# Kernel optimization log

Hardware: AMD Instinct MI355X
Metric: run time of the kernel (lower is better)

Reference implementation:

```python
import jax, jax.numpy as jnp
import numpy as np
from jax import lax

THRESH = 0.8
LENS = 0.4
DECAY = 0.2
LOG_SIG_MIN, LOG_SIG_MAX = -20.0, 2.0
WINS = 15

@jax.custom_vjp
def act_fun(x):
    return (x > THRESH).astype(x.dtype)

def _act_fwd(x):
    return act_fun(x), x

def _act_bwd(x, g):
    return (g * (jnp.abs(x - THRESH) < LENS).astype(g.dtype),)

act_fun.defvjp(_act_fwd, _act_bwd)

B, NIN, HID, NACT = 2048, 512, 1024, 32

def _xavier(key, out_d, in_d):
    lim = jnp.sqrt(6.0 / (in_d + out_d)).astype(jnp.float32)
    return jax.random.uniform(key, (out_d, in_d), jnp.float32, -lim, lim)

def setup_inputs() -> dict:
    key = jax.random.key(0)
    ks = jax.random.split(key, 12)
    inp = {
        'state': jax.random.normal(ks[0], (B, 5, NIN), jnp.float32),
        'w1': _xavier(ks[1], HID, NIN), 'b1': jnp.zeros((HID,), jnp.float32),
        'w2': _xavier(ks[2], HID, NIN), 'b2': jnp.zeros((HID,), jnp.float32),
        'w3': _xavier(ks[3], HID, NIN), 'b3': jnp.zeros((HID,), jnp.float32),
        'wl': _xavier(ks[4], 1, 3), 'bl': jnp.zeros((1,), jnp.float32),
        'w11': _xavier(ks[5], HID, 4 * HID), 'b11': jnp.zeros((HID,), jnp.float32),
        'w12': _xavier(ks[6], HID, HID), 'b12': jnp.zeros((HID,), jnp.float32),
        'w21': _xavier(ks[7], HID, 4 * HID), 'b21': jnp.zeros((HID,), jnp.float32),
        'w22': _xavier(ks[8], HID, HID), 'b22': jnp.zeros((HID,), jnp.float32),
        'wm': _xavier(ks[9], NACT, HID), 'bm': jnp.zeros((NACT,), jnp.float32),
        'ws': _xavier(ks[10], NACT, HID), 'bs': jnp.zeros((NACT,), jnp.float32),
    }
    return inp

def _policy_forward(state, w1, b1, w2, b2, w3, b3, wl, bl,
                    w11, b11, w12, b12, w21, b21, w22, b22, wm, bm, ws, bs):
    batch = state.shape[0]
    hid = w1.shape[0]
    seq = jnp.repeat(state, 3, axis=1)
    mem0 = jnp.zeros((batch, hid, 4), state.dtype)
    sp0 = jnp.zeros((batch, hid, 4), state.dtype)

    def step(carry, x_t):
        mem, spike = carry
        i1 = x_t @ w1.T + b1  # [B, HID]
        i2 = x_t @ w2.T + b2
        i3 = x_t @ w3.T + b3
        inner = jnp.einsum('bck,k->bc', mem[:, :, :3], wl[0]) + bl[0]
        inp_all = jnp.stack([i1, i2, i3, inner], axis=-1)  # [B, HID, 4]
        mem1 = mem * DECAY * (1.0 - spike) + inp_all
        sp1 = act_fun(mem1)
        return (mem1, sp1), sp1

    _, spikes = lax.scan(step, (mem0, sp0), jnp.swapaxes(seq, 0, 1))  # [T,B,HID,4]
    spikes = jnp.transpose(spikes, (1, 0, 2, 3)).reshape(batch, WINS, hid * 4)
    x = jnp.mean(spikes, axis=1)  # [B, 4*HID]

    x1 = jax.nn.relu(x @ w11.T + b11)
    x1 = jax.nn.relu(x1 @ w12.T + b12)
    mean = x1 @ wm.T + bm

    x2 = jax.nn.relu(x @ w21.T + b21)
    x2 = jax.nn.relu(x2 @ w22.T + b22)
    log_std = jnp.clip(x2 @ ws.T + bs, LOG_SIG_MIN, LOG_SIG_MAX)
    return mean, log_std

def reference(state, w1, b1, w2, b2, w3, b3, wl, bl,
              w11, b11, w12, b12, w21, b21, w22, b22, wm, bm, ws, bs):
    return _policy_forward(state, w1, b1, w2, b2, w3, b3, wl, bl,
                           w11, b11, w12, b12, w21, b21, w22, b22, wm, bm, ws, bs)
```

## Files before the change

kernel.cpp:

```cpp
#include <hip/hip_runtime.h>
#include <cstddef>
#include <cstdint>

#define THRESH 0.8f
#define DECAY  0.2f

typedef unsigned short ushort_t;
typedef __attribute__((ext_vector_type(8))) short bf16x8;
typedef __attribute__((ext_vector_type(4))) float f32x4;

__device__ __forceinline__ ushort_t f2bf(float f) {
    union { float f; unsigned u; } v; v.f = f;
    unsigned r = v.u + 0x7FFFu + ((v.u >> 16) & 1u);
    return (ushort_t)(r >> 16);
}
__device__ __forceinline__ float bf2f(ushort_t h) {
    union { unsigned u; float f; } v; v.u = ((unsigned)h) << 16;
    return v.f;
}
__device__ __forceinline__ float blo(unsigned u) {
    union { unsigned x; float f; } v; v.x = u << 16; return v.f;
}
__device__ __forceinline__ float bhi(unsigned u) {
    union { unsigned x; float f; } v; v.x = u & 0xFFFF0000u; return v.f;
}

__device__ __forceinline__ void gload16(const void* g, void* l) {
    __builtin_amdgcn_global_load_lds(
        (const __attribute__((address_space(1))) void*)g,
        (__attribute__((address_space(3))) void*)l,
        16, 0, 0);
}

__global__ __launch_bounds__(512) void cur_gemm512(
    const ushort_t* __restrict__ Ah, const ushort_t* __restrict__ Al,
    const ushort_t* __restrict__ Wh, const ushort_t* __restrict__ Wl,
    const float* __restrict__ bias, float* __restrict__ C,
    int K, int ldc)
{
    __shared__ ushort_t sA[2][128 * 32];
    __shared__ ushort_t sW[2][128 * 32];

    const int t = threadIdx.x;
    const int mBase = blockIdx.x * 128;
    const int nBase = blockIdx.y * 128;

    const int lane = t & 63;
    const int wv = t >> 6;
    const int wm = (wv & 1) * 64;
    const int wn = (wv >> 1) * 32;
    const int fr = lane & 15;
    const int fq = lane >> 4;

    const int r0 = t >> 2;
    const int cc = (t & 3) * 8;

    f32x4 acc[4][2];
#pragma unroll
    for (int i = 0; i < 4; i++)
#pragma unroll
        for (int j = 0; j < 2; j++) {
            f32x4 z = {0.f, 0.f, 0.f, 0.f};
            acc[i][j] = z;
        }

    for (int k0 = 0; k0 < K; k0 += 32) {
        const int lin = t * 8;
        gload16(&Ah[(size_t)(mBase + r0) * K + k0 + cc], &sA[0][lin]);
        gload16(&Wh[(size_t)(nBase + r0) * K + k0 + cc], &sW[0][lin]);
        gload16(&Al[(size_t)(mBase + r0) * K + k0 + cc], &sA[1][lin]);
        gload16(&Wl[(size_t)(nBase + r0) * K + k0 + cc], &sW[1][lin]);
        __syncthreads();

        bf16x8 af[4][2], wf[2][2];
#pragma unroll
        for (int s = 0; s < 2; s++) {
#pragma unroll
            for (int i = 0; i < 4; i++)
                af[i][s] = *(const bf16x8*)&sA[s][(wm + i * 16 + fr) * 32 + fq * 8];
#pragma unroll
            for (int j = 0; j < 2; j++)
                wf[j][s] = *(const bf16x8*)&sW[s][(wn + j * 16 + fr) * 32 + fq * 8];
        }
#pragma unroll
        for (int i = 0; i < 4; i++)
#pragma unroll
            for (int j = 0; j < 2; j++) {
                acc[i][j] = __builtin_amdgcn_mfma_f32_16x16x32_bf16(af[i][0], wf[j][0], acc[i][j], 0, 0, 0);
                acc[i][j] = __builtin_amdgcn_mfma_f32_16x16x32_bf16(af[i][0], wf[j][1], acc[i][j], 0, 0, 0);
                acc[i][j] = __builtin_amdgcn_mfma_f32_16x16x32_bf16(af[i][1], wf[j][0], acc[i][j], 0, 0, 0);
            }
        __syncthreads();
    }

#pragma unroll
    for (int j = 0; j < 2; j++) {
        const int col = nBase + wn + j * 16 + fr;
        const float bv = bias[col];
#pragma unroll
        for (int i = 0; i < 4; i++)
#pragma unroll
            for (int r = 0; r < 4; r++) {
                const int row = mBase + wm + i * 16 + fq * 4 + r;
                C[(size_t)row * ldc + col] = acc[i][j][r] + bv;
            }
    }
}

__global__ __launch_bounds__(256) void mlp_gemm256(
    const ushort_t* __restrict__ A, const ushort_t* __restrict__ W,
    float* __restrict__ C,
    int N, int K, int lda, int ldw, int ldc, int aHalfOff,
    size_t sliceStride)
{
    __shared__ ushort_t sA[128 * 32];
    __shared__ ushort_t sW[128 * 32];

    const int t = threadIdx.x;
    const int mBase = blockIdx.x * 128;
    const int nBase = blockIdx.y * 128;
    const int kOff = blockIdx.z * K;
    const int aOff = (2 * nBase >= N) ? aHalfOff : 0;
    float* Cz = C + (size_t)blockIdx.z * sliceStride;

    const int lane = t & 63;
    const int wv = t >> 6;
    const int wm = (wv & 1) * 64;
    const int wn = (wv >> 1) * 64;
    const int fr = lane & 15;
    const int fq = lane >> 4;

    const int r0 = t >> 2;
    const int cc = (t & 3) * 8;

    f32x4 acc[4][4];
#pragma unroll
    for (int i = 0; i < 4; i++)
#pragma unroll
        for (int j = 0; j < 4; j++) {
            f32x4 z = {0.f, 0.f, 0.f, 0.f};
            acc[i][j] = z;
        }

    for (int k0 = 0; k0 < K; k0 += 32) {
        gload16(&A[(size_t)(mBase + r0) * lda + aOff + kOff + k0 + cc], &sA[t * 8]);
        gload16(&A[(size_t)(mBase + 64 + r0) * lda + aOff + kOff + k0 + cc], &sA[2048 + t * 8]);
        gload16(&W[(size_t)(nBase + r0) * ldw + kOff + k0 + cc], &sW[t * 8]);
        gload16(&W[(size_t)(nBase + 64 + r0) * ldw + kOff + k0 + cc], &sW[2048 + t * 8]);
        __syncthreads();

        bf16x8 af[4], wf[4];
#pragma unroll
        for (int i = 0; i < 4; i++) {
            af[i] = *(const bf16x8*)&sA[(wm + i * 16 + fr) * 32 + fq * 8];
            wf[i] = *(const bf16x8*)&sW[(wn + i * 16 + fr) * 32 + fq * 8];
        }
#pragma unroll
        for (int i = 0; i < 4; i++)
#pragma unroll
            for (int j = 0; j < 4; j++)
                acc[i][j] = __builtin_amdgcn_mfma_f32_16x16x32_bf16(af[i], wf[j], acc[i][j], 0, 0, 0);
        __syncthreads();
    }

#pragma unroll
    for (int j = 0; j < 4; j++) {
        const int col = nBase + wn + j * 16 + fr;
#pragma unroll
        for (int i = 0; i < 4; i++)
#pragma unroll
            for (int r = 0; r < 4; r++) {
                const int row = mBase + wm + i * 16 + fq * 4 + r;
                Cz[(size_t)row * ldc + col] = acc[i][j][r];
            }
    }
}

template <int S>
__global__ __launch_bounds__(256) void reduce_relu(
    const float* __restrict__ part, const float* __restrict__ bias,
    ushort_t* __restrict__ out, int N, size_t MN)
{
    const size_t e = ((size_t)blockIdx.x * 256 + threadIdx.x) * 4;
    if (e >= MN) return;
    float4 a = *(const float4*)&part[e];
#pragma unroll
    for (int s = 1; s < S; s++) {
        const float4 b = *(const float4*)&part[s * MN + e];
        a.x += b.x; a.y += b.y; a.z += b.z; a.w += b.w;
    }
    const int n = (int)(e & (size_t)(N - 1));
    const float4 bv = *(const float4*)&bias[n];
    ushort4 o;
    o.x = f2bf(fmaxf(a.x + bv.x, 0.f));
    o.y = f2bf(fmaxf(a.y + bv.y, 0.f));
    o.z = f2bf(fmaxf(a.z + bv.z, 0.f));
    o.w = f2bf(fmaxf(a.w + bv.w, 0.f));
    *(ushort4*)&out[e] = o;
}

__global__ __launch_bounds__(256) void recur_kernel(
    const float* __restrict__ cur, const float* __restrict__ wl,
    const float* __restrict__ bl, ushort_t* __restrict__ x)
{
    const int idx = blockIdx.x * 256 + threadIdx.x;
    const int b = idx >> 10, c = idx & 1023;
    const float wl0 = wl[0], wl1 = wl[1], wl2 = wl[2], bl0 = bl[0];
    float m0 = 0, m1 = 0, m2 = 0, m3 = 0;
    float s0 = 0, s1 = 0, s2 = 0, s3 = 0;
#pragma unroll
    for (int f = 0; f < 5; f++) {
        const float* p = cur + (size_t)(b * 5 + f) * 3072 + c;
        const float i1 = p[0], i2 = p[1024], i3 = p[2048];
#pragma unroll
        for (int rep = 0; rep < 3; rep++) {
            const float inner = m0 * wl0 + m1 * wl1 + m2 * wl2 + bl0;
            const float n0 = i1 + ((m0 > THRESH) ? 0.f : DECAY * m0);
            const float n1 = i2 + ((m1 > THRESH) ? 0.f : DECAY * m1);
            const float n2 = i3 + ((m2 > THRESH) ? 0.f : DECAY * m2);
            const float n3 = inner + ((m3 > THRESH) ? 0.f : DECAY * m3);
            m0 = n0; m1 = n1; m2 = n2; m3 = n3;
            s0 += (n0 > THRESH) ? 1.f : 0.f;
            s1 += (n1 > THRESH) ? 1.f : 0.f;
            s2 += (n2 > THRESH) ? 1.f : 0.f;
            s3 += (n3 > THRESH) ? 1.f : 0.f;
        }
    }
    const float inv = 1.f / 15.f;
    ushort4 o;
    o.x = f2bf(s0 * inv); o.y = f2bf(s1 * inv);
    o.z = f2bf(s2 * inv); o.w = f2bf(s3 * inv);
    *(ushort4*)&x[(size_t)b * 4096 + c * 4] = o;
}

__device__ __forceinline__ void do_split4(const float4* src, ushort4* hi,
                                          ushort4* lo, int base, int t) {
#pragma unroll
    for (int p = 0; p < 4; p++) {
        const int i = base * 1024 + p * 256 + t;
        const float4 v = src[i];
        ushort4 h, l;
        h.x = f2bf(v.x); l.x = f2bf(v.x - bf2f(h.x));
        h.y = f2bf(v.y); l.y = f2bf(v.y - bf2f(h.y));
        h.z = f2bf(v.z); l.z = f2bf(v.z - bf2f(h.z));
        h.w = f2bf(v.w); l.w = f2bf(v.w - bf2f(h.w));
        hi[i] = h; lo[i] = l;
    }
}
__device__ __forceinline__ void do_cvt4(const float4* src, ushort4* dst,
                                        int base, int t) {
#pragma unroll
    for (int p = 0; p < 4; p++) {
        const int i = base * 1024 + p * 256 + t;
        const float4 v = src[i];
        ushort4 h;
        h.x = f2bf(v.x); h.y = f2bf(v.y); h.z = f2bf(v.z); h.w = f2bf(v.w);
        dst[i] = h;
    }
}

__global__ __launch_bounds__(256) void prep_kernel(
    const float* __restrict__ state,
    const float* __restrict__ w1, const float* __restrict__ w2,
    const float* __restrict__ w3,
    const float* __restrict__ w11, const float* __restrict__ w21,
    const float* __restrict__ w12, const float* __restrict__ w22,
    const float* __restrict__ b1, const float* __restrict__ b2,
    const float* __restrict__ b3, const float* __restrict__ b11,
    const float* __restrict__ b21, const float* __restrict__ b12,
    const float* __restrict__ b22,
    ushort_t* __restrict__ sh, ushort_t* __restrict__ sl,
    ushort_t* __restrict__ wh123, ushort_t* __restrict__ wl123,
    ushort_t* __restrict__ w1b, ushort_t* __restrict__ w2b,
    float* __restrict__ b123, float* __restrict__ bb1, float* __restrict__ bb2)
{
    const int bid = blockIdx.x;
    const int t = threadIdx.x;
    if (bid < 1280) {
        do_split4((const float4*)state, (ushort4*)sh, (ushort4*)sl, bid, t);
    } else if (bid < 1408) {
        do_split4((const float4*)w1, (ushort4*)wh123, (ushort4*)wl123, bid - 1280, t);
    } else if (bid < 1536) {
        do_split4((const float4*)w2, (ushort4*)(wh123 + 524288),
                  (ushort4*)(wl123 + 524288), bid - 1408, t);
    } else if (bid < 1664) {
        do_split4((const float4*)w3, (ushort4*)(wh123 + 1048576),
                  (ushort4*)(wl123 + 1048576), bid - 1536, t);
    } else if (bid < 2688) {
        do_cvt4((const float4*)w11, (ushort4*)w1b, bid - 1664, t);
    } else if (bid < 3712) {
        do_cvt4((const float4*)w21, (ushort4*)(w1b + 4194304), bid - 2688, t);
    } else if (bid < 3968) {
        do_cvt4((const float4*)w12, (ushort4*)w2b, bid - 3712, t);
    } else if (bid < 4224) {
        do_cvt4((const float4*)w22, (ushort4*)(w2b + 1048576), bid - 3968, t);
    } else {
#pragma unroll
        for (int p = 0; p < 4; p++) {
            const int i = p * 256 + t;
            b123[i] = b1[i]; b123[1024 + i] = b2[i]; b123[2048 + i] = b3[i];
            bb1[i] = b11[i]; bb1[1024 + i] = b21[i];
            bb2[i] = b12[i]; bb2[1024 + i] = b22[i];
        }
    }
}

__global__ __launch_bounds__(256) void head_kernel(
    const ushort_t* __restrict__ h, const float* __restrict__ wm,
    const float* __restrict__ bm, const float* __restrict__ ws,
    const float* __restrict__ bs, float* __restrict__ out)
{
    const int t = threadIdx.x;
    const int branch = blockIdx.x >> 8;
    const int n = t & 31;
    const int b = (blockIdx.x & 255) * 8 + (t >> 5);
    const ushort_t* hr = h + (size_t)b * 2048 + branch * 1024;
    const float* wr = (branch ? ws : wm) + (size_t)n * 1024;
    float s = 0.f;
#pragma unroll 4
    for (int k = 0; k < 1024; k += 8) {
        const uint4 hv = *(const uint4*)&hr[k];
        const float4 w0 = *(const float4*)&wr[k];
        const float4 w1 = *(const float4*)&wr[k + 4];
        s += blo(hv.x) * w0.x + bhi(hv.x) * w0.y
           + blo(hv.y) * w0.z + bhi(hv.y) * w0.w
           + blo(hv.z) * w1.x + bhi(hv.z) * w1.y
           + blo(hv.w) * w1.z + bhi(hv.w) * w1.w;
    }
    s += (branch ? bs : bm)[n];
    if (branch) s = fminf(fmaxf(s, -20.f), 2.f);
    out[(size_t)branch * 65536 + (size_t)b * 32 + n] = s;
}

extern "C" void kernel_launch(void* const* d_in, const int* in_sizes, int n_in,
                              void* d_out, int out_size, void* d_ws, size_t ws_size,
                              hipStream_t stream)
{
    const float* state = (const float*)d_in[0];
    const float* w1  = (const float*)d_in[1];  const float* b1  = (const float*)d_in[2];
    const float* w2  = (const float*)d_in[3];  const float* b2  = (const float*)d_in[4];
    const float* w3  = (const float*)d_in[5];  const float* b3  = (const float*)d_in[6];
    const float* wl  = (const float*)d_in[7];  const float* bl  = (const float*)d_in[8];
    const float* w11 = (const float*)d_in[9];  const float* b11 = (const float*)d_in[10];
    const float* w12 = (const float*)d_in[11]; const float* b12 = (const float*)d_in[12];
    const float* w21 = (const float*)d_in[13]; const float* b21 = (const float*)d_in[14];
    const float* w22 = (const float*)d_in[15]; const float* b22 = (const float*)d_in[16];
    const float* wm  = (const float*)d_in[17]; const float* bm  = (const float*)d_in[18];
    const float* ws  = (const float*)d_in[19]; const float* bs  = (const float*)d_in[20];
    float* out = (float*)d_out;

    char* wp = (char*)d_ws;
    float*    cur   = (float*)wp;     wp += (size_t)10240 * 3072 * 4;
    ushort_t* sh    = (ushort_t*)wp;  wp += (size_t)10240 * 512 * 2;
    ushort_t* sl    = (ushort_t*)wp;  wp += (size_t)10240 * 512 * 2;
    ushort_t* wh123 = (ushort_t*)wp;  wp += (size_t)3072 * 512 * 2;
    ushort_t* wl123 = (ushort_t*)wp;  wp += (size_t)3072 * 512 * 2;
    ushort_t* xb    = (ushort_t*)wp;  wp += (size_t)2048 * 4096 * 2;
    ushort_t* w1b   = (ushort_t*)wp;  wp += (size_t)2048 * 4096 * 2;
    ushort_t* w2b   = (ushort_t*)wp;  wp += (size_t)2048 * 1024 * 2;
    ushort_t* h1    = (ushort_t*)wp;  wp += (size_t)2048 * 2048 * 2;
    ushort_t* h2    = (ushort_t*)wp;  wp += (size_t)2048 * 2048 * 2;
    float*    b123  = (float*)wp;     wp += 3072 * 4;
    float*    bb1   = (float*)wp;     wp += 2048 * 4;
    float*    bb2   = (float*)wp;     wp += 2048 * 4;

    const size_t MN = (size_t)2048 * 2048;

    prep_kernel<<<4225, 256, 0, stream>>>(
        state, w1, w2, w3, w11, w21, w12, w22,
        b1, b2, b3, b11, b21, b12, b22,
        sh, sl, wh123, wl123, w1b, w2b, b123, bb1, bb2);

    cur_gemm512<<<dim3(80, 24), 512, 0, stream>>>(
        sh, sl, wh123, wl123, b123, cur, 512, 3072);

    recur_kernel<<<8192, 256, 0, stream>>>(cur, wl, bl, xb);

    mlp_gemm256<<<dim3(16, 16, 4), 256, 0, stream>>>(
        xb, w1b, cur, 2048, 1024, 4096, 4096, 2048, 0, MN);
    reduce_relu<4><<<4096, 256, 0, stream>>>(cur, bb1, h1, 2048, MN);

    mlp_gemm256<<<dim3(16, 16, 2), 256, 0, stream>>>(
        h1, w2b, cur, 2048, 512, 2048, 1024, 2048, 1024, MN);
    reduce_relu<2><<<4096, 256, 0, stream>>>(cur, bb2, h2, 2048, MN);

    head_kernel<<<512, 256, 0, stream>>>(h2, wm, bm, ws, bs, out);
}
```

Before: 413.8 us.

## Quantize first MLP layer to int8 MFMA and drop split-K reductions

The spike-count activations are now stored as exact int8 counts (0..15), and w11/w21 are quantized per row to int8 with a scale that also folds in the 1/15 mean. The first MLP GEMM uses int8 MFMA with a fused scale, bias and ReLU epilogue. Both MLP GEMMs drop split-K and the separate reduce_relu kernels and write bf16 directly. This halves operand bytes and removes the fp32 partial-sum traffic, but per-row int8 weight quantization adds approximation error, and without split-K each GEMM launches only 256 blocks.

```diff
diff --git a/kernel.cpp b/kernel.cpp
--- a/kernel.cpp
+++ b/kernel.cpp
@@ -8,6 +8,7 @@
 typedef unsigned short ushort_t;
 typedef __attribute__((ext_vector_type(8))) short bf16x8;
 typedef __attribute__((ext_vector_type(4))) float f32x4;
+typedef __attribute__((ext_vector_type(4))) int i32x4;
 
 __device__ __forceinline__ ushort_t f2bf(float f) {
     union { float f; unsigned u; } v; v.f = f;
@@ -107,21 +108,17 @@
     }
 }
 
-__global__ __launch_bounds__(256) void mlp_gemm256(
-    const ushort_t* __restrict__ A, const ushort_t* __restrict__ W,
-    float* __restrict__ C,
-    int N, int K, int lda, int ldw, int ldc, int aHalfOff,
-    size_t sliceStride)
-{
-    __shared__ ushort_t sA[128 * 32];
-    __shared__ ushort_t sW[128 * 32];
+__global__ __launch_bounds__(256) void mlp1_i8(
+    const signed char* __restrict__ A, const signed char* __restrict__ W,
+    const float* __restrict__ wsc, const float* __restrict__ bias,
+    ushort_t* __restrict__ C)
+{
+    __shared__ signed char sA[128 * 32];
+    __shared__ signed char sW[128 * 32];
 
     const int t = threadIdx.x;
     const int mBase = blockIdx.x * 128;
     const int nBase = blockIdx.y * 128;
-    const int kOff = blockIdx.z * K;
-    const int aOff = (2 * nBase >= N) ? aHalfOff : 0;
-    float* Cz = C + (size_t)blockIdx.z * sliceStride;
 
     const int lane = t & 63;
     const int wv = t >> 6;
@@ -130,6 +127,73 @@
     const int fr = lane & 15;
     const int fq = lane >> 4;
 
+    const int r0 = t >> 1;
+    const int cc = (t & 1) * 16;
+
+    i32x4 acc[4][4];
+#pragma unroll
+    for (int i = 0; i < 4; i++)
+#pragma unroll
+        for (int j = 0; j < 4; j++) {
+            i32x4 z = {0, 0, 0, 0};
+            acc[i][j] = z;
+        }
+
+    for (int k0 = 0; k0 < 4096; k0 += 32) {
+        gload16(&A[(size_t)(mBase + r0) * 4096 + k0 + cc], &sA[t * 16]);
+        gload16(&W[(size_t)(nBase + r0) * 4096 + k0 + cc], &sW[t * 16]);
+        __syncthreads();
+
+        long aL[4], wL[4];
+#pragma unroll
+        for (int i = 0; i < 4; i++) {
+            aL[i] = *(const long*)&sA[(wm + i * 16 + fr) * 32 + fq * 8];
+            wL[i] = *(const long*)&sW[(wn + i * 16 + fr) * 32 + fq * 8];
+        }
+#pragma unroll
+        for (int i = 0; i < 4; i++)
+#pragma unroll
+            for (int j = 0; j < 4; j++)
+                acc[i][j] = __builtin_amdgcn_mfma_i32_16x16x32_i8(aL[i], wL[j], acc[i][j], 0, 0, 0);
+        __syncthreads();
+    }
+
+#pragma unroll
+    for (int j = 0; j < 4; j++) {
+        const int col = nBase + wn + j * 16 + fr;
+        const float sc = wsc[col];
+        const float bv = bias[col];
+#pragma unroll
+        for (int i = 0; i < 4; i++)
+#pragma unroll
+            for (int r = 0; r < 4; r++) {
+                const int row = mBase + wm + i * 16 + fq * 4 + r;
+                const float v = (float)acc[i][j][r] * sc + bv;
+                C[(size_t)row * 2048 + col] = f2bf(fmaxf(v, 0.f));
+            }
+    }
+}
+
+__global__ __launch_bounds__(256) void mlp2_bf16(
+    const ushort_t* __restrict__ A, const ushort_t* __restrict__ W,
+    const float* __restrict__ bias, ushort_t* __restrict__ C,
+    int N, int K, int lda, int ldw, int ldc, int aHalfOff)
+{
+    __shared__ ushort_t sA[128 * 32];
+    __shared__ ushort_t sW[128 * 32];
+
+    const int t = threadIdx.x;
+    const int mBase = blockIdx.x * 128;
+    const int nBase = blockIdx.y * 128;
+    const int aOff = (2 * nBase >= N) ? aHalfOff : 0;
+
+    const int lane = t & 63;
+    const int wv = t >> 6;
+    const int wm = (wv & 1) * 64;
+    const int wn = (wv >> 1) * 64;
+    const int fr = lane & 15;
+    const int fq = lane >> 4;
+
     const int r0 = t >> 2;
     const int cc = (t & 3) * 8;
 
@@ -143,10 +207,10 @@
         }
 
     for (int k0 = 0; k0 < K; k0 += 32) {
-        gload16(&A[(size_t)(mBase + r0) * lda + aOff + kOff + k0 + cc], &sA[t * 8]);
-        gload16(&A[(size_t)(mBase + 64 + r0) * lda + aOff + kOff + k0 + cc], &sA[2048 + t * 8]);
-        gload16(&W[(size_t)(nBase + r0) * ldw + kOff + k0 + cc], &sW[t * 8]);
-        gload16(&W[(size_t)(nBase + 64 + r0) * ldw + kOff + k0 + cc], &sW[2048 + t * 8]);
+        gload16(&A[(size_t)(mBase + r0) * lda + aOff + k0 + cc], &sA[t * 8]);
+        gload16(&A[(size_t)(mBase + 64 + r0) * lda + aOff + k0 + cc], &sA[2048 + t * 8]);
+        gload16(&W[(size_t)(nBase + r0) * ldw + k0 + cc], &sW[t * 8]);
+        gload16(&W[(size_t)(nBase + 64 + r0) * ldw + k0 + cc], &sW[2048 + t * 8]);
         __syncthreads();
 
         bf16x8 af[4], wf[4];
@@ -166,48 +230,26 @@
 #pragma unroll
     for (int j = 0; j < 4; j++) {
         const int col = nBase + wn + j * 16 + fr;
+        const float bv = bias[col];
 #pragma unroll
         for (int i = 0; i < 4; i++)
 #pragma unroll
             for (int r = 0; r < 4; r++) {
                 const int row = mBase + wm + i * 16 + fq * 4 + r;
-                Cz[(size_t)row * ldc + col] = acc[i][j][r];
+                C[(size_t)row * ldc + col] = f2bf(fmaxf(acc[i][j][r] + bv, 0.f));
             }
     }
-}
-
-template <int S>
-__global__ __launch_bounds__(256) void reduce_relu(
-    const float* __restrict__ part, const float* __restrict__ bias,
-    ushort_t* __restrict__ out, int N, size_t MN)
-{
-    const size_t e = ((size_t)blockIdx.x * 256 + threadIdx.x) * 4;
-    if (e >= MN) return;
-    float4 a = *(const float4*)&part[e];
-#pragma unroll
-    for (int s = 1; s < S; s++) {
-        const float4 b = *(const float4*)&part[s * MN + e];
-        a.x += b.x; a.y += b.y; a.z += b.z; a.w += b.w;
-    }
-    const int n = (int)(e & (size_t)(N - 1));
-    const float4 bv = *(const float4*)&bias[n];
-    ushort4 o;
-    o.x = f2bf(fmaxf(a.x + bv.x, 0.f));
-    o.y = f2bf(fmaxf(a.y + bv.y, 0.f));
-    o.z = f2bf(fmaxf(a.z + bv.z, 0.f));
-    o.w = f2bf(fmaxf(a.w + bv.w, 0.f));
-    *(ushort4*)&out[e] = o;
 }
 
 __global__ __launch_bounds__(256) void recur_kernel(
     const float* __restrict__ cur, const float* __restrict__ wl,
-    const float* __restrict__ bl, ushort_t* __restrict__ x)
+    const float* __restrict__ bl, signed char* __restrict__ x)
 {
     const int idx = blockIdx.x * 256 + threadIdx.x;
     const int b = idx >> 10, c = idx & 1023;
     const float wl0 = wl[0], wl1 = wl[1], wl2 = wl[2], bl0 = bl[0];
     float m0 = 0, m1 = 0, m2 = 0, m3 = 0;
-    float s0 = 0, s1 = 0, s2 = 0, s3 = 0;
+    int s0 = 0, s1 = 0, s2 = 0, s3 = 0;
 #pragma unroll
     for (int f = 0; f < 5; f++) {
         const float* p = cur + (size_t)(b * 5 + f) * 3072 + c;
@@ -220,17 +262,14 @@
             const float n2 = i3 + ((m2 > THRESH) ? 0.f : DECAY * m2);
             const float n3 = inner + ((m3 > THRESH) ? 0.f : DECAY * m3);
             m0 = n0; m1 = n1; m2 = n2; m3 = n3;
-            s0 += (n0 > THRESH) ? 1.f : 0.f;
-            s1 += (n1 > THRESH) ? 1.f : 0.f;
-            s2 += (n2 > THRESH) ? 1.f : 0.f;
-            s3 += (n3 > THRESH) ? 1.f : 0.f;
-        }
-    }
-    const float inv = 1.f / 15.f;
-    ushort4 o;
-    o.x = f2bf(s0 * inv); o.y = f2bf(s1 * inv);
-    o.z = f2bf(s2 * inv); o.w = f2bf(s3 * inv);
-    *(ushort4*)&x[(size_t)b * 4096 + c * 4] = o;
+            s0 += (n0 > THRESH); s1 += (n1 > THRESH);
+            s2 += (n2 > THRESH); s3 += (n3 > THRESH);
+        }
+    }
+    uchar4 o;
+    o.x = (unsigned char)s0; o.y = (unsigned char)s1;
+    o.z = (unsigned char)s2; o.w = (unsigned char)s3;
+    *(uchar4*)&x[(size_t)b * 4096 + c * 4] = o;
 }
 
 __device__ __forceinline__ void do_split4(const float4* src, ushort4* hi,
@@ -257,6 +296,11 @@
         h.x = f2bf(v.x); h.y = f2bf(v.y); h.z = f2bf(v.z); h.w = f2bf(v.w);
         dst[i] = h;
     }
+}
+__device__ __forceinline__ int q8(float x, float inv) {
+    int q = (int)rintf(x * inv);
+    q = q > 127 ? 127 : (q < -127 ? -127 : q);
+    return q & 0xff;
 }
 
 __global__ __launch_bounds__(256) void prep_kernel(
@@ -271,7 +315,8 @@
     const float* __restrict__ b22,
     ushort_t* __restrict__ sh, ushort_t* __restrict__ sl,
     ushort_t* __restrict__ wh123, ushort_t* __restrict__ wl123,
-    ushort_t* __restrict__ w1b, ushort_t* __restrict__ w2b,
+    signed char* __restrict__ w1q, float* __restrict__ wsc,
+    ushort_t* __restrict__ w2b,
     float* __restrict__ b123, float* __restrict__ bb1, float* __restrict__ bb2)
 {
     const int bid = blockIdx.x;
@@ -286,10 +331,34 @@
     } else if (bid < 1664) {
         do_split4((const float4*)w3, (ushort4*)(wh123 + 1048576),
                   (ushort4*)(wl123 + 1048576), bid - 1536, t);
-    } else if (bid < 2688) {
-        do_cvt4((const float4*)w11, (ushort4*)w1b, bid - 1664, t);
     } else if (bid < 3712) {
-        do_cvt4((const float4*)w21, (ushort4*)(w1b + 4194304), bid - 2688, t);
+        const int r = bid - 1664;
+        const float* src = (r < 1024) ? (w11 + (size_t)r * 4096)
+                                      : (w21 + (size_t)(r - 1024) * 4096);
+        __shared__ float red[256];
+        float4 v[4];
+        float lmax = 0.f;
+#pragma unroll
+        for (int p = 0; p < 4; p++) {
+            v[p] = ((const float4*)src)[t * 4 + p];
+            lmax = fmaxf(lmax, fmaxf(fmaxf(fabsf(v[p].x), fabsf(v[p].y)),
+                                     fmaxf(fabsf(v[p].z), fabsf(v[p].w))));
+        }
+        red[t] = lmax;
+        __syncthreads();
+        for (int s = 128; s > 0; s >>= 1) {
+            if (t < s) red[t] = fmaxf(red[t], red[t + s]);
+            __syncthreads();
+        }
+        const float gmax = fmaxf(red[0], 1e-30f);
+        const float inv = 127.0f / gmax;
+        int4 o;
+        o.x = q8(v[0].x, inv) | (q8(v[0].y, inv) << 8) | (q8(v[0].z, inv) << 16) | (q8(v[0].w, inv) << 24);
+        o.y = q8(v[1].x, inv) | (q8(v[1].y, inv) << 8) | (q8(v[1].z, inv) << 16) | (q8(v[1].w, inv) << 24);
+        o.z = q8(v[2].x, inv) | (q8(v[2].y, inv) << 8) | (q8(v[2].z, inv) << 16) | (q8(v[2].w, inv) << 24);
+        o.w = q8(v[3].x, inv) | (q8(v[3].y, inv) << 8) | (q8(v[3].z, inv) << 16) | (q8(v[3].w, inv) << 24);
+        ((int4*)(w1q + (size_t)r * 4096))[t] = o;
+        if (t == 0) wsc[r] = gmax / (127.0f * 15.0f);
     } else if (bid < 3968) {
         do_cvt4((const float4*)w12, (ushort4*)w2b, bid - 3712, t);
     } else if (bid < 4224) {
@@ -350,39 +419,35 @@
     float* out = (float*)d_out;
 
     char* wp = (char*)d_ws;
-    float*    cur   = (float*)wp;     wp += (size_t)10240 * 3072 * 4;
-    ushort_t* sh    = (ushort_t*)wp;  wp += (size_t)10240 * 512 * 2;
-    ushort_t* sl    = (ushort_t*)wp;  wp += (size_t)10240 * 512 * 2;
-    ushort_t* wh123 = (ushort_t*)wp;  wp += (size_t)3072 * 512 * 2;
-    ushort_t* wl123 = (ushort_t*)wp;  wp += (size_t)3072 * 512 * 2;
-    ushort_t* xb    = (ushort_t*)wp;  wp += (size_t)2048 * 4096 * 2;
-    ushort_t* w1b   = (ushort_t*)wp;  wp += (size_t)2048 * 4096 * 2;
-    ushort_t* w2b   = (ushort_t*)wp;  wp += (size_t)2048 * 1024 * 2;
-    ushort_t* h1    = (ushort_t*)wp;  wp += (size_t)2048 * 2048 * 2;
-    ushort_t* h2    = (ushort_t*)wp;  wp += (size_t)2048 * 2048 * 2;
-    float*    b123  = (float*)wp;     wp += 3072 * 4;
-    float*    bb1   = (float*)wp;     wp += 2048 * 4;
-    float*    bb2   = (float*)wp;     wp += 2048 * 4;
-
-    const size_t MN = (size_t)2048 * 2048;
+    float*       cur   = (float*)wp;       wp += (size_t)10240 * 3072 * 4;
+    ushort_t*    sh    = (ushort_t*)wp;    wp += (size_t)10240 * 512 * 2;
+    ushort_t*    sl    = (ushort_t*)wp;    wp += (size_t)10240 * 512 * 2;
+    ushort_t*    wh123 = (ushort_t*)wp;    wp += (size_t)3072 * 512 * 2;
+    ushort_t*    wl123 = (ushort_t*)wp;    wp += (size_t)3072 * 512 * 2;
+    signed char* xb    = (signed char*)wp; wp += (size_t)2048 * 4096;
+    signed char* w1q   = (signed char*)wp; wp += (size_t)2048 * 4096;
+    ushort_t*    w2b   = (ushort_t*)wp;    wp += (size_t)2048 * 1024 * 2;
+    ushort_t*    h1    = (ushort_t*)wp;    wp += (size_t)2048 * 2048 * 2;
+    ushort_t*    h2    = (ushort_t*)wp;    wp += (size_t)2048 * 2048 * 2;
+    float*       wsc   = (float*)wp;       wp += 2048 * 4;
+    float*       b123  = (float*)wp;       wp += 3072 * 4;
+    float*       bb1   = (float*)wp;       wp += 2048 * 4;
+    float*       bb2   = (float*)wp;       wp += 2048 * 4;
 
     prep_kernel<<<4225, 256, 0, stream>>>(
         state, w1, w2, w3, w11, w21, w12, w22,
         b1, b2, b3, b11, b21, b12, b22,
-        sh, sl, wh123, wl123, w1b, w2b, b123, bb1, bb2);
+        sh, sl, wh123, wl123, w1q, wsc, w2b, b123, bb1, bb2);
 
     cur_gemm512<<<dim3(80, 24), 512, 0, stream>>>(
         sh, sl, wh123, wl123, b123, cur, 512, 3072);
 
     recur_kernel<<<8192, 256, 0, stream>>>(cur, wl, bl, xb);
 
-    mlp_gemm256<<<dim3(16, 16, 4), 256, 0, stream>>>(
-        xb, w1b, cur, 2048, 1024, 4096, 4096, 2048, 0, MN);
-    reduce_relu<4><<<4096, 256, 0, stream>>>(cur, bb1, h1, 2048, MN);
-
-    mlp_gemm256<<<dim3(16, 16, 2), 256, 0, stream>>>(
-        h1, w2b, cur, 2048, 512, 2048, 1024, 2048, 1024, MN);
-    reduce_relu<2><<<4096, 256, 0, stream>>>(cur, bb2, h2, 2048, MN);
+    mlp1_i8<<<dim3(16, 16), 256, 0, stream>>>(xb, w1q, wsc, bb1, h1);
+
+    mlp2_bf16<<<dim3(16, 16), 256, 0, stream>>>(
+        h1, w2b, bb2, h2, 2048, 1024, 2048, 1024, 2048, 1024);
 
     head_kernel<<<512, 256, 0, stream>>>(h2, wm, bm, ws, bs, out);
 }
```

Measured after the change: 436.6 us. 5.5% more time.
